# Kernel optimization log

Measured on AMD Instinct MI355X. Metric: run time of the kernel, lower is better.

## Reference

```python
import jax, jax.numpy as jnp
import numpy as np

SH_C0 = 0.28209479177387814
SH_C1 = 0.4886025119029199
SH_C2 = (1.0925484305920792, -1.0925484305920792, 0.31539156525252005, -1.0925484305920792, 0.5462742152960396)
SH_C3 = (-0.5900435899266435, 2.890611442640554, -0.4570457994644658, 0.3731763325901154, -0.4570457994644658, 1.445305721320277, -0.5900435899266435)

BG = 128  # gaussians per compositing block


def quat_to_rot(q):
    # q: [N,4] normalized quaternion (w,x,y,z) -> [N,3,3]
    w, x, y, z = q[:, 0], q[:, 1], q[:, 2], q[:, 3]
    R = jnp.stack([
        1 - 2 * (y * y + z * z), 2 * (x * y - w * z), 2 * (x * z + w * y),
        2 * (x * y + w * z), 1 - 2 * (x * x + z * z), 2 * (y * z - w * x),
        2 * (x * z - w * y), 2 * (y * z + w * x), 1 - 2 * (x * x + y * y)],
        axis=-1)
    return R.reshape(-1, 3, 3)


def eval_sh(sh, d):
    # sh: [N,16,3] degree-3 SH coeffs; d: [N,3] unit view dirs -> [N,3] rgb
    x, y, z = d[:, 0:1], d[:, 1:2], d[:, 2:3]
    xx, yy, zz = x * x, y * y, z * z
    xy, yz, xz = x * y, y * z, x * z
    res = SH_C0 * sh[:, 0]
    res = res - SH_C1 * y * sh[:, 1] + SH_C1 * z * sh[:, 2] - SH_C1 * x * sh[:, 3]
    res = (res + SH_C2[0] * xy * sh[:, 4] + SH_C2[1] * yz * sh[:, 5]
           + SH_C2[2] * (2 * zz - xx - yy) * sh[:, 6]
           + SH_C2[3] * xz * sh[:, 7] + SH_C2[4] * (xx - yy) * sh[:, 8])
    res = (res + SH_C3[0] * y * (3 * xx - yy) * sh[:, 9] + SH_C3[1] * xy * z * sh[:, 10]
           + SH_C3[2] * y * (4 * zz - xx - yy) * sh[:, 11]
           + SH_C3[3] * z * (2 * zz - 3 * xx - 3 * yy) * sh[:, 12]
           + SH_C3[4] * x * (4 * zz - xx - yy) * sh[:, 13]
           + SH_C3[5] * z * (xx - yy) * sh[:, 14] + SH_C3[6] * x * (xx - 3 * yy) * sh[:, 15])
    return res


def gs_forward(pws, shs, alphas_raw, scales_raw, rots_raw, us, Rcw, tcw, intr, height, width):
    fx, fy, cx, cy = intr[0], intr[1], intr[2], intr[3]
    N = pws.shape[0]
    HW = height * width

    # activations (GSModel.forward)
    alphas = jax.nn.sigmoid(alphas_raw[:, 0])          # [N]
    scales = jnp.exp(scales_raw)                       # [N,3]
    rots = rots_raw / jnp.linalg.norm(rots_raw, axis=1, keepdims=True)

    # gsc.project
    pcs = pws @ Rcw.T + tcw                            # [N,3] camera frame
    depth = pcs[:, 2]
    zs = jnp.where(depth > 0.2, depth, 1.0)            # safe divide for culled pts
    u = jnp.stack([fx * pcs[:, 0] / zs + cx, fy * pcs[:, 1] / zs + cy], axis=-1)
    # the `us` input is a grad-capture dummy; forward value comes from projection
    u = u + us - jax.lax.stop_gradient(us)

    # gsc.computeCov3D: Cov3d = (R S)(R S)^T
    R = quat_to_rot(rots)
    M = R * scales[:, None, :]
    cov3d = M @ jnp.swapaxes(M, 1, 2)                  # [N,3,3]

    # gsc.computeCov2D: cov2d = J W Cov3d W^T J^T + 0.3 I
    tanfx = width / (2.0 * fx)
    tanfy = height / (2.0 * fy)
    tx = jnp.clip(pcs[:, 0] / zs, -1.3 * tanfx, 1.3 * tanfx) * zs
    ty = jnp.clip(pcs[:, 1] / zs, -1.3 * tanfy, 1.3 * tanfy) * zs
    zero = jnp.zeros_like(zs)
    J = jnp.stack([
        fx / zs, zero, -fx * tx / (zs * zs),
        zero, fy / zs, -fy * ty / (zs * zs)], axis=-1).reshape(N, 2, 3)
    T = jnp.einsum('nij,jk->nik', J, Rcw)              # [N,2,3]
    cov2d = jnp.einsum('nij,njk,nlk->nil', T, cov3d, T)
    cov2d = cov2d + 0.3 * jnp.eye(2, dtype=cov2d.dtype)
    a, b, c = cov2d[:, 0, 0], cov2d[:, 0, 1], cov2d[:, 1, 1]
    det = a * c - b * b
    valid = (depth > 0.2) & (det > 0)
    det_s = jnp.where(valid, det, 1.0)

    # gsc.inverseCov2D: conic + screen-space radius (areas)
    cinv = jnp.stack([c / det_s, -b / det_s, a / det_s], axis=-1)  # [N,3]
    mid = 0.5 * (a + c)
    lam = mid + jnp.sqrt(jnp.maximum(mid * mid - det, 0.1))
    radius = jnp.where(valid, jnp.ceil(3.0 * jnp.sqrt(lam)), 0.0)
    areas = jnp.stack([radius, radius], axis=-1)       # [N,2]

    # gsc.sh2Color
    twc = -Rcw.T @ tcw
    dirs = pws - twc
    dirs = dirs / jnp.linalg.norm(dirs, axis=1, keepdims=True)
    colors = jnp.maximum(eval_sh(shs.reshape(N, 16, 3), dirs) + 0.5, 0.0)  # [N,3]

    # gsc.splat: depth-sorted front-to-back alpha compositing over all pixels
    order = jnp.argsort(depth)
    nb = N // BG
    u_s = u[order].reshape(nb, BG, 2)
    cinv_s = cinv[order].reshape(nb, BG, 3)
    al_s = alphas[order].reshape(nb, BG)
    col_s = colors[order].reshape(nb, BG, 3)
    val_s = valid[order].reshape(nb, BG)

    ys, xs = jnp.meshgrid(jnp.arange(height, dtype=jnp.float32),
                          jnp.arange(width, dtype=jnp.float32), indexing='ij')
    px = xs.ravel()
    py = ys.ravel()

    @jax.checkpoint
    def body(carry, blk):
        logT, acc = carry                              # [HW], [3,HW]
        ub, cb, ab, colb, vb = blk
        dx = px[None, :] - ub[:, 0:1]                  # [BG,HW]
        dy = py[None, :] - ub[:, 1:2]
        power = -0.5 * (cb[:, 0:1] * dx * dx + cb[:, 2:3] * dy * dy) - cb[:, 1:2] * dx * dy
        alp = jnp.minimum(0.99, ab[:, None] * jnp.exp(power))
        alp = jnp.where((power <= 0) & (alp >= 1.0 / 255.0) & vb[:, None], alp, 0.0)
        l1m = jnp.log1p(-alp)
        cs = jnp.cumsum(l1m, axis=0)
        logT_i = logT[None, :] + jnp.concatenate(
            [jnp.zeros((1, HW), l1m.dtype), cs[:-1]], axis=0)  # exclusive transmittance
        Ti = jnp.exp(logT_i)
        w = jnp.where(Ti > 1e-4, alp * Ti, 0.0)        # early-termination at tau<1e-4
        acc = acc + jnp.einsum('gp,gc->cp', w, colb)
        return (logT + cs[-1], acc), None

    init = (jnp.zeros(HW, dtype=jnp.float32), jnp.zeros((3, HW), dtype=jnp.float32))
    (_, acc), _ = jax.lax.scan(body, init, (u_s, cinv_s, al_s, col_s, val_s))
    image = acc.reshape(3, height, width)
    return image, areas


def setup_inputs() -> dict:
    key = jax.random.key(0)
    ks = jax.random.split(key, 6)
    N, H, W = 8192, 256, 256
    pws = jax.random.normal(ks[0], (N, 3), jnp.float32) * 2.0 + jnp.array([0.0, 0.0, 6.0])
    shs = jax.random.normal(ks[1], (N, 48), jnp.float32) * 0.3
    alphas_raw = jax.random.normal(ks[2], (N, 1), jnp.float32)
    scales_raw = jax.random.normal(ks[3], (N, 3), jnp.float32) * 0.3 - 3.0
    rots_raw = jax.random.normal(ks[4], (N, 4), jnp.float32)
    us = jnp.zeros((N, 2), jnp.float32)
    Rcw = jnp.eye(3, dtype=jnp.float32)
    tcw = jnp.zeros((3,), jnp.float32)
    intr = jnp.array([400.0, 400.0, 128.0, 128.0], jnp.float32)  # fx, fy, cx, cy
    return {"pws": pws, "shs": shs, "alphas_raw": alphas_raw, "scales_raw": scales_raw,
            "rots_raw": rots_raw, "us": us, "Rcw": Rcw, "tcw": tcw, "intr": intr,
            "height": H, "width": W}


def reference(pws, shs, alphas_raw, scales_raw, rots_raw, us, Rcw, tcw, intr, height, width):
    return gs_forward(pws, shs, alphas_raw, scales_raw, rots_raw, us, Rcw, tcw, intr, height, width)
```

## Files before the change

### kernel.cpp

```cpp
#include <hip/hip_runtime.h>

__global__ __launch_bounds__(256) void k_pre(
    const float* __restrict__ pws, const float* __restrict__ shs,
    const float* __restrict__ alphas_raw, const float* __restrict__ scales_raw,
    const float* __restrict__ rots_raw, const float* __restrict__ Rcw,
    const float* __restrict__ tcw, const float* __restrict__ intr,
    int N, int W, int H, float* __restrict__ areas,
    unsigned long long* __restrict__ keys, unsigned* __restrict__ rank,
    float* __restrict__ P)
{
    int i = blockIdx.x * 256 + threadIdx.x;
    if (i >= N) return;
    rank[i] = 0u;

    float R00=Rcw[0],R01=Rcw[1],R02=Rcw[2];
    float R10=Rcw[3],R11=Rcw[4],R12=Rcw[5];
    float R20=Rcw[6],R21=Rcw[7],R22=Rcw[8];
    float t0=tcw[0],t1=tcw[1],t2=tcw[2];
    float fx=intr[0],fy=intr[1],cx=intr[2],cy=intr[3];

    float pwx=pws[i*3+0], pwy=pws[i*3+1], pwz=pws[i*3+2];
    float pcx = R00*pwx + R01*pwy + R02*pwz + t0;
    float pcy = R10*pwx + R11*pwy + R12*pwz + t1;
    float pcz = R20*pwx + R21*pwy + R22*pwz + t2;
    float depth = pcz;
    float zs = (depth > 0.2f) ? depth : 1.0f;
    float u0 = fx * pcx / zs + cx;
    float u1 = fy * pcy / zs + cy;

    float qw=rots_raw[i*4+0], qx=rots_raw[i*4+1], qy=rots_raw[i*4+2], qz=rots_raw[i*4+3];
    float qn = sqrtf(qw*qw + qx*qx + qy*qy + qz*qz);
    qw/=qn; qx/=qn; qy/=qn; qz/=qn;
    float s0 = expf(scales_raw[i*3+0]);
    float s1 = expf(scales_raw[i*3+1]);
    float s2 = expf(scales_raw[i*3+2]);

    float xx=qx*qx, yy=qy*qy, zq=qz*qz;
    float xy=qx*qy, xz=qx*qz, yz=qy*qz;
    float wx=qw*qx, wy=qw*qy, wz=qw*qz;
    float r00=1.f-2.f*(yy+zq), r01=2.f*(xy-wz),     r02=2.f*(xz+wy);
    float r10=2.f*(xy+wz),     r11=1.f-2.f*(xx+zq), r12=2.f*(yz-wx);
    float r20=2.f*(xz-wy),     r21=2.f*(yz+wx),     r22=1.f-2.f*(xx+yy);

    float m00=r00*s0, m01=r01*s1, m02=r02*s2;
    float m10=r10*s0, m11=r11*s1, m12=r12*s2;
    float m20=r20*s0, m21=r21*s1, m22=r22*s2;
    float V00=m00*m00+m01*m01+m02*m02;
    float V01=m00*m10+m01*m11+m02*m12;
    float V02=m00*m20+m01*m21+m02*m22;
    float V11=m10*m10+m11*m11+m12*m12;
    float V12=m10*m20+m11*m21+m12*m22;
    float V22=m20*m20+m21*m21+m22*m22;

    float tanfx = (float)W / (2.f*fx), tanfy = (float)H / (2.f*fy);
    float limx = 1.3f*tanfx, limy = 1.3f*tanfy;
    float txl = fminf(fmaxf(pcx/zs, -limx), limx) * zs;
    float tyl = fminf(fmaxf(pcy/zs, -limy), limy) * zs;
    float iz = 1.f/zs, iz2 = iz*iz;
    float J00 = fx*iz, J02 = -fx*txl*iz2;
    float J11 = fy*iz, J12 = -fy*tyl*iz2;

    float T00=J00*R00+J02*R20, T01=J00*R01+J02*R21, T02=J00*R02+J02*R22;
    float T10=J11*R10+J12*R20, T11=J11*R11+J12*R21, T12=J11*R12+J12*R22;
    float A0=T00*V00+T01*V01+T02*V02;
    float A1=T00*V01+T01*V11+T02*V12;
    float A2=T00*V02+T01*V12+T02*V22;
    float B0=T10*V00+T11*V01+T12*V02;
    float B1=T10*V01+T11*V11+T12*V12;
    float B2=T10*V02+T11*V12+T12*V22;
    float ca = A0*T00+A1*T01+A2*T02 + 0.3f;
    float cb = A0*T10+A1*T11+A2*T12;
    float cc = B0*T10+B1*T11+B2*T12 + 0.3f;

    float det = ca*cc - cb*cb;
    bool valid = (depth > 0.2f) && (det > 0.f);
    float det_s = valid ? det : 1.f;
    float dinv = 1.f/det_s;
    float ci0 =  cc*dinv, ci1 = -cb*dinv, ci2 = ca*dinv;
    float mid = 0.5f*(ca+cc);
    float lam = mid + sqrtf(fmaxf(mid*mid - det, 0.1f));
    float radius = valid ? ceilf(3.f*sqrtf(lam)) : 0.f;
    areas[2*i+0] = radius;
    areas[2*i+1] = radius;

    float alpha = 1.f/(1.f + expf(-alphas_raw[i]));

    float tw0 = -(R00*t0 + R10*t1 + R20*t2);
    float tw1 = -(R01*t0 + R11*t1 + R21*t2);
    float tw2 = -(R02*t0 + R12*t1 + R22*t2);
    float dx_=pwx-tw0, dy_=pwy-tw1, dz_=pwz-tw2;
    float dn = sqrtf(dx_*dx_+dy_*dy_+dz_*dz_);
    float x=dx_/dn, y=dy_/dn, z=dz_/dn;
    float sxx=x*x, syy=y*y, szz=z*z;
    float sxy=x*y, syz=y*z, sxz=x*z;
    const float* sh = shs + i*48;
    float col[3];
    #pragma unroll
    for (int c = 0; c < 3; ++c) {
        float res = 0.28209479177387814f*sh[0*3+c];
        res += -0.4886025119029199f*y*sh[1*3+c]
             +  0.4886025119029199f*z*sh[2*3+c]
             + -0.4886025119029199f*x*sh[3*3+c];
        res +=  1.0925484305920792f*sxy*sh[4*3+c]
             + -1.0925484305920792f*syz*sh[5*3+c]
             +  0.31539156525252005f*(2.f*szz-sxx-syy)*sh[6*3+c]
             + -1.0925484305920792f*sxz*sh[7*3+c]
             +  0.5462742152960396f*(sxx-syy)*sh[8*3+c];
        res += -0.5900435899266435f*y*(3.f*sxx-syy)*sh[9*3+c]
             +  2.890611442640554f*sxy*z*sh[10*3+c]
             + -0.4570457994644658f*y*(4.f*szz-sxx-syy)*sh[11*3+c]
             +  0.3731763325901154f*z*(2.f*szz-3.f*sxx-3.f*syy)*sh[12*3+c]
             + -0.4570457994644658f*x*(4.f*szz-sxx-syy)*sh[13*3+c]
             +  1.445305721320277f*z*(sxx-syy)*sh[14*3+c]
             + -0.5900435899266435f*x*(sxx-3.f*syy)*sh[15*3+c];
        col[c] = fmaxf(res + 0.5f, 0.f);
    }

    float rc2;
    if (!valid || 255.f*alpha < 0.999f) {
        rc2 = -1.f;
    } else {
        float r2 = 2.f*lam*logf(255.f*alpha);
        float r  = sqrtf(fmaxf(r2, 0.f)) + 1.f;
        rc2 = r*r;
    }

    P[0*N+i]=u0;  P[1*N+i]=u1;  P[2*N+i]=ci0; P[3*N+i]=ci1; P[4*N+i]=ci2;
    P[5*N+i]=alpha; P[6*N+i]=col[0]; P[7*N+i]=col[1]; P[8*N+i]=col[2];
    P[9*N+i]=rc2;

    unsigned ud = __float_as_uint(depth);
    ud = (ud & 0x80000000u) ? ~ud : (ud | 0x80000000u);
    keys[i] = ((unsigned long long)ud << 32) | (unsigned)i;
}

#define JC 512
__global__ __launch_bounds__(256) void k_rank(
    const unsigned long long* __restrict__ keys, int N,
    unsigned* __restrict__ rank)
{
    __shared__ unsigned long long sk[JC];
    const int j0 = blockIdx.y * JC;
    for (int t = threadIdx.x; t < JC; t += 256) {
        int j = j0 + t;
        sk[t] = (j < N) ? keys[j] : ~0ull;
    }
    __syncthreads();

    const int i0 = blockIdx.x * 512 + threadIdx.x;
    const int i1 = i0 + 256;
    unsigned long long my0 = (i0 < N) ? keys[i0] : 0ull;
    unsigned long long my1 = (i1 < N) ? keys[i1] : 0ull;

    int c0 = 0, c1 = 0;
    const ulonglong2* sk2 = (const ulonglong2*)sk;
    #pragma unroll 4
    for (int t = 0; t < JC/2; ++t) {
        ulonglong2 kk = sk2[t];
        c0 += (kk.x < my0) ? 1 : 0;
        c0 += (kk.y < my0) ? 1 : 0;
        c1 += (kk.x < my1) ? 1 : 0;
        c1 += (kk.y < my1) ? 1 : 0;
    }
    if (i0 < N) atomicAdd(&rank[i0], (unsigned)c0);
    if (i1 < N) atomicAdd(&rank[i1], (unsigned)c1);
}

__global__ __launch_bounds__(256) void k_scatter(
    const unsigned* __restrict__ rank, const float* __restrict__ Pun,
    float* __restrict__ Pso, float4* __restrict__ cull, int N)
{
    int i = blockIdx.x * 256 + threadIdx.x;
    if (i >= N) return;
    int s = (int)rank[i];
    cull[s] = make_float4(Pun[0*N+i], Pun[1*N+i], Pun[9*N+i], 0.f);
    Pso[0*N+s] = Pun[2*N+i];
    Pso[1*N+s] = Pun[3*N+i];
    Pso[2*N+s] = Pun[4*N+i];
    Pso[3*N+s] = Pun[5*N+i];
    Pso[4*N+s] = Pun[6*N+i];
    Pso[5*N+s] = Pun[7*N+i];
    Pso[6*N+s] = Pun[8*N+i];
}

__global__ __launch_bounds__(256) void k_render(
    const float* __restrict__ P, const float4* __restrict__ cull,
    int N, int W, int H, float* __restrict__ out)
{
    const int tid = threadIdx.x;
    const int tilesX = (W + 15) >> 4;
    const int tX = blockIdx.x % tilesX, tY = blockIdx.x / tilesX;
    const int ix = (tX << 4) + (tid & 15);
    const int iy = (tY << 4) + (tid >> 4);
    const bool inb = (ix < W) && (iy < H);
    const float pxf = (float)ix, pyf = (float)iy;
    const float tx0 = (float)(tX << 4), ty0 = (float)(tY << 4);
    int tx1i = (tX << 4) + 15; if (tx1i > W-1) tx1i = W-1;
    int ty1i = (tY << 4) + 15; if (ty1i > H-1) ty1i = H-1;
    const float tx1 = (float)tx1i, ty1 = (float)ty1i;

    float T = inb ? 1.f : 0.f;
    float aR = 0.f, aG = 0.f, aB = 0.f;

    __shared__ float sU0[256], sU1[256], sC0[256], sC1[256], sC2[256];
    __shared__ float sA[256], sCR[256], sCG[256], sCB[256];
    __shared__ unsigned long long sMask[4];

    const int wave = tid >> 6, lane = tid & 63;

    for (int base = 0; base < N; base += 256) {
        int g = base + tid;
        bool ov = false;
        float u0=0.f,u1=0.f,c0=0.f,c1=0.f,c2=0.f,al=0.f,cr=0.f,cg=0.f,cbl=0.f;
        if (g < N) {
            float4 cu = cull[g];
            u0 = cu.x; u1 = cu.y;
            float cxp = fminf(fmaxf(u0, tx0), tx1);
            float cyp = fminf(fmaxf(u1, ty0), ty1);
            float ddx = u0 - cxp, ddy = u1 - cyp;
            ov = (ddx*ddx + ddy*ddy) <= cu.z;
            if (ov) {
                c0 = P[0*N+g]; c1 = P[1*N+g]; c2 = P[2*N+g]; al = P[3*N+g];
                cr = P[4*N+g]; cg = P[5*N+g]; cbl = P[6*N+g];
            }
        }
        unsigned long long m = __ballot(ov);
        if (lane == 0) sMask[wave] = m;
        __syncthreads();
        int cnt = 0, off = 0;
        #pragma unroll
        for (int w2 = 0; w2 < 4; ++w2) {
            int pc = __popcll(sMask[w2]);
            if (w2 < wave) off += pc;
            cnt += pc;
        }
        if (ov) {
            int pos = off + __popcll(m & ((1ull << lane) - 1ull));
            sU0[pos]=u0; sU1[pos]=u1; sC0[pos]=c0; sC1[pos]=c1; sC2[pos]=c2;
            sA[pos]=al; sCR[pos]=cr; sCB[pos]=cbl; sCG[pos]=cg;
        }
        __syncthreads();

        for (int e = 0; e < cnt; ++e) {
            float gu0=sU0[e], gu1=sU1[e];
            float gc0=sC0[e], gc1=sC1[e], gc2=sC2[e];
            float ga=sA[e], gr=sCR[e], gg=sCG[e], gb=sCB[e];
            float ddx = pxf - gu0, ddy = pyf - gu1;
            float power = -0.5f*(gc0*ddx*ddx + gc2*ddy*ddy) - gc1*ddx*ddy;
            float alp = fminf(0.99f, ga * __expf(power));
            alp = (power <= 0.f && alp >= (1.0f/255.0f)) ? alp : 0.f;
            float w = (T > 0.0001f) ? alp * T : 0.f;
            aR = fmaf(w, gr, aR);
            aG = fmaf(w, gg, aG);
            aB = fmaf(w, gb, aB);
            T = T - T * alp;
        }
        int done = (T <= 0.0001f) ? 1 : 0;
        if (__syncthreads_and(done)) break;
    }

    if (inb) {
        int p = iy * W + ix;
        int HWp = W * H;
        out[p] = aR; out[HWp + p] = aG; out[2*HWp + p] = aB;
    }
}

extern "C" void kernel_launch(void* const* d_in, const int* in_sizes, int n_in,
                              void* d_out, int out_size, void* d_ws, size_t ws_size,
                              hipStream_t stream) {
    const float* pws        = (const float*)d_in[0];
    const float* shs        = (const float*)d_in[1];
    const float* alphas_raw = (const float*)d_in[2];
    const float* scales_raw = (const float*)d_in[3];
    const float* rots_raw   = (const float*)d_in[4];
    const float* Rcw        = (const float*)d_in[6];
    const float* tcw        = (const float*)d_in[7];
    const float* intr       = (const float*)d_in[8];

    const int N  = in_sizes[0] / 3;
    const int HW = (out_size - 2 * N) / 3;
    int W = 1; while ((long long)W * W < (long long)HW) ++W;
    const int H = HW / W;

    float* out   = (float*)d_out;
    float* areas = out + 3 * HW;

    char* ws = (char*)d_ws;
    unsigned long long* keys = (unsigned long long*)ws;
    unsigned* rank = (unsigned*)(ws + (size_t)N * 8);
    float* Pun = (float*)(ws + (size_t)N * 12);
    float* Pso = Pun + (size_t)10 * N;
    float4* cullv = (float4*)(Pso + (size_t)7 * N);

    int gsN = (N + 255) / 256;
    k_pre<<<gsN, 256, 0, stream>>>(pws, shs, alphas_raw, scales_raw, rots_raw,
                                   Rcw, tcw, intr, N, W, H, areas, keys, rank, Pun);
    dim3 rgrid((N + 511) / 512, (N + JC - 1) / JC);
    k_rank<<<rgrid, 256, 0, stream>>>(keys, N, rank);
    k_scatter<<<gsN, 256, 0, stream>>>(rank, Pun, Pso, cullv, N);
    int tiles = ((W + 15) / 16) * ((H + 15) / 16);
    k_render<<<tiles, 256, 0, stream>>>(Pso, cullv, N, W, H, out);
}
```

Before: 130.9 us.

## Fuse all stages into one cooperative kernel and split rendering by depth halves

The four separate launches (preprocess, rank, scatter, render) become one cooperative kernel of 512 blocks, separated by grid-wide syncs, to remove launch gaps. Rendering now gives each 16x16 tile two blocks, each compositing one half of the depth-sorted Gaussians. The back half's transmittance and colour are written to a buffer and merged front-to-back after a final grid sync, doubling parallelism for the 256 tiles. The cost is four grid barriers, fewer threads in the preprocess and scatter phases (16 per block), and the back half doing work that early termination would otherwise skip.

```diff
diff --git a/kernel.cpp b/kernel.cpp
--- a/kernel.cpp
+++ b/kernel.cpp
@@ -1,268 +1,298 @@
 #include <hip/hip_runtime.h>
-
-__global__ __launch_bounds__(256) void k_pre(
+#include <hip/hip_cooperative_groups.h>
+
+namespace cg = cooperative_groups;
+
+#define NBLK 512
+#define BT   256
+
+union SharedU {
+    unsigned long long sk[512];
+    struct {
+        float U0[256], U1[256], C0[256], C1[256], C2[256];
+        float A[256], CR[256], CG[256], CB[256];
+        unsigned long long mask[4];
+    } r;
+};
+
+__global__ void __launch_bounds__(BT, 2) k_fused(
     const float* __restrict__ pws, const float* __restrict__ shs,
     const float* __restrict__ alphas_raw, const float* __restrict__ scales_raw,
     const float* __restrict__ rots_raw, const float* __restrict__ Rcw,
     const float* __restrict__ tcw, const float* __restrict__ intr,
-    int N, int W, int H, float* __restrict__ areas,
+    int N, int W, int H,
+    float* __restrict__ out, float* __restrict__ areas,
     unsigned long long* __restrict__ keys, unsigned* __restrict__ rank,
-    float* __restrict__ P)
+    float* __restrict__ Pun, float* __restrict__ Pso,
+    float4* __restrict__ cull, float4* __restrict__ seg1buf)
 {
-    int i = blockIdx.x * 256 + threadIdx.x;
-    if (i >= N) return;
-    rank[i] = 0u;
-
-    float R00=Rcw[0],R01=Rcw[1],R02=Rcw[2];
-    float R10=Rcw[3],R11=Rcw[4],R12=Rcw[5];
-    float R20=Rcw[6],R21=Rcw[7],R22=Rcw[8];
-    float t0=tcw[0],t1=tcw[1],t2=tcw[2];
-    float fx=intr[0],fy=intr[1],cx=intr[2],cy=intr[3];
-
-    float pwx=pws[i*3+0], pwy=pws[i*3+1], pwz=pws[i*3+2];
-    float pcx = R00*pwx + R01*pwy + R02*pwz + t0;
-    float pcy = R10*pwx + R11*pwy + R12*pwz + t1;
-    float pcz = R20*pwx + R21*pwy + R22*pwz + t2;
-    float depth = pcz;
-    float zs = (depth > 0.2f) ? depth : 1.0f;
-    float u0 = fx * pcx / zs + cx;
-    float u1 = fy * pcy / zs + cy;
-
-    float qw=rots_raw[i*4+0], qx=rots_raw[i*4+1], qy=rots_raw[i*4+2], qz=rots_raw[i*4+3];
-    float qn = sqrtf(qw*qw + qx*qx + qy*qy + qz*qz);
-    qw/=qn; qx/=qn; qy/=qn; qz/=qn;
-    float s0 = expf(scales_raw[i*3+0]);
-    float s1 = expf(scales_raw[i*3+1]);
-    float s2 = expf(scales_raw[i*3+2]);
-
-    float xx=qx*qx, yy=qy*qy, zq=qz*qz;
-    float xy=qx*qy, xz=qx*qz, yz=qy*qz;
-    float wx=qw*qx, wy=qw*qy, wz=qw*qz;
-    float r00=1.f-2.f*(yy+zq), r01=2.f*(xy-wz),     r02=2.f*(xz+wy);
-    float r10=2.f*(xy+wz),     r11=1.f-2.f*(xx+zq), r12=2.f*(yz-wx);
-    float r20=2.f*(xz-wy),     r21=2.f*(yz+wx),     r22=1.f-2.f*(xx+yy);
-
-    float m00=r00*s0, m01=r01*s1, m02=r02*s2;
-    float m10=r10*s0, m11=r11*s1, m12=r12*s2;
-    float m20=r20*s0, m21=r21*s1, m22=r22*s2;
-    float V00=m00*m00+m01*m01+m02*m02;
-    float V01=m00*m10+m01*m11+m02*m12;
-    float V02=m00*m20+m01*m21+m02*m22;
-    float V11=m10*m10+m11*m11+m12*m12;
-    float V12=m10*m20+m11*m21+m12*m22;
-    float V22=m20*m20+m21*m21+m22*m22;
-
-    float tanfx = (float)W / (2.f*fx), tanfy = (float)H / (2.f*fy);
-    float limx = 1.3f*tanfx, limy = 1.3f*tanfy;
-    float txl = fminf(fmaxf(pcx/zs, -limx), limx) * zs;
-    float tyl = fminf(fmaxf(pcy/zs, -limy), limy) * zs;
-    float iz = 1.f/zs, iz2 = iz*iz;
-    float J00 = fx*iz, J02 = -fx*txl*iz2;
-    float J11 = fy*iz, J12 = -fy*tyl*iz2;
-
-    float T00=J00*R00+J02*R20, T01=J00*R01+J02*R21, T02=J00*R02+J02*R22;
-    float T10=J11*R10+J12*R20, T11=J11*R11+J12*R21, T12=J11*R12+J12*R22;
-    float A0=T00*V00+T01*V01+T02*V02;
-    float A1=T00*V01+T01*V11+T02*V12;
-    float A2=T00*V02+T01*V12+T02*V22;
-    float B0=T10*V00+T11*V01+T12*V02;
-    float B1=T10*V01+T11*V11+T12*V12;
-    float B2=T10*V02+T11*V12+T12*V22;
-    float ca = A0*T00+A1*T01+A2*T02 + 0.3f;
-    float cb = A0*T10+A1*T11+A2*T12;
-    float cc = B0*T10+B1*T11+B2*T12 + 0.3f;
-
-    float det = ca*cc - cb*cb;
-    bool valid = (depth > 0.2f) && (det > 0.f);
-    float det_s = valid ? det : 1.f;
-    float dinv = 1.f/det_s;
-    float ci0 =  cc*dinv, ci1 = -cb*dinv, ci2 = ca*dinv;
-    float mid = 0.5f*(ca+cc);
-    float lam = mid + sqrtf(fmaxf(mid*mid - det, 0.1f));
-    float radius = valid ? ceilf(3.f*sqrtf(lam)) : 0.f;
-    areas[2*i+0] = radius;
-    areas[2*i+1] = radius;
-
-    float alpha = 1.f/(1.f + expf(-alphas_raw[i]));
-
-    float tw0 = -(R00*t0 + R10*t1 + R20*t2);
-    float tw1 = -(R01*t0 + R11*t1 + R21*t2);
-    float tw2 = -(R02*t0 + R12*t1 + R22*t2);
-    float dx_=pwx-tw0, dy_=pwy-tw1, dz_=pwz-tw2;
-    float dn = sqrtf(dx_*dx_+dy_*dy_+dz_*dz_);
-    float x=dx_/dn, y=dy_/dn, z=dz_/dn;
-    float sxx=x*x, syy=y*y, szz=z*z;
-    float sxy=x*y, syz=y*z, sxz=x*z;
-    const float* sh = shs + i*48;
-    float col[3];
-    #pragma unroll
-    for (int c = 0; c < 3; ++c) {
-        float res = 0.28209479177387814f*sh[0*3+c];
-        res += -0.4886025119029199f*y*sh[1*3+c]
-             +  0.4886025119029199f*z*sh[2*3+c]
-             + -0.4886025119029199f*x*sh[3*3+c];
-        res +=  1.0925484305920792f*sxy*sh[4*3+c]
-             + -1.0925484305920792f*syz*sh[5*3+c]
-             +  0.31539156525252005f*(2.f*szz-sxx-syy)*sh[6*3+c]
-             + -1.0925484305920792f*sxz*sh[7*3+c]
-             +  0.5462742152960396f*(sxx-syy)*sh[8*3+c];
-        res += -0.5900435899266435f*y*(3.f*sxx-syy)*sh[9*3+c]
-             +  2.890611442640554f*sxy*z*sh[10*3+c]
-             + -0.4570457994644658f*y*(4.f*szz-sxx-syy)*sh[11*3+c]
-             +  0.3731763325901154f*z*(2.f*szz-3.f*sxx-3.f*syy)*sh[12*3+c]
-             + -0.4570457994644658f*x*(4.f*szz-sxx-syy)*sh[13*3+c]
-             +  1.445305721320277f*z*(sxx-syy)*sh[14*3+c]
-             + -0.5900435899266435f*x*(sxx-3.f*syy)*sh[15*3+c];
-        col[c] = fmaxf(res + 0.5f, 0.f);
-    }
-
-    float rc2;
-    if (!valid || 255.f*alpha < 0.999f) {
-        rc2 = -1.f;
-    } else {
-        float r2 = 2.f*lam*logf(255.f*alpha);
-        float r  = sqrtf(fmaxf(r2, 0.f)) + 1.f;
-        rc2 = r*r;
-    }
-
-    P[0*N+i]=u0;  P[1*N+i]=u1;  P[2*N+i]=ci0; P[3*N+i]=ci1; P[4*N+i]=ci2;
-    P[5*N+i]=alpha; P[6*N+i]=col[0]; P[7*N+i]=col[1]; P[8*N+i]=col[2];
-    P[9*N+i]=rc2;
-
-    unsigned ud = __float_as_uint(depth);
-    ud = (ud & 0x80000000u) ? ~ud : (ud | 0x80000000u);
-    keys[i] = ((unsigned long long)ud << 32) | (unsigned)i;
-}
-
-#define JC 512
-__global__ __launch_bounds__(256) void k_rank(
-    const unsigned long long* __restrict__ keys, int N,
-    unsigned* __restrict__ rank)
-{
-    __shared__ unsigned long long sk[JC];
-    const int j0 = blockIdx.y * JC;
-    for (int t = threadIdx.x; t < JC; t += 256) {
-        int j = j0 + t;
-        sk[t] = (j < N) ? keys[j] : ~0ull;
-    }
-    __syncthreads();
-
-    const int i0 = blockIdx.x * 512 + threadIdx.x;
-    const int i1 = i0 + 256;
-    unsigned long long my0 = (i0 < N) ? keys[i0] : 0ull;
-    unsigned long long my1 = (i1 < N) ? keys[i1] : 0ull;
-
-    int c0 = 0, c1 = 0;
-    const ulonglong2* sk2 = (const ulonglong2*)sk;
-    #pragma unroll 4
-    for (int t = 0; t < JC/2; ++t) {
-        ulonglong2 kk = sk2[t];
-        c0 += (kk.x < my0) ? 1 : 0;
-        c0 += (kk.y < my0) ? 1 : 0;
-        c1 += (kk.x < my1) ? 1 : 0;
-        c1 += (kk.y < my1) ? 1 : 0;
-    }
-    if (i0 < N) atomicAdd(&rank[i0], (unsigned)c0);
-    if (i1 < N) atomicAdd(&rank[i1], (unsigned)c1);
-}
-
-__global__ __launch_bounds__(256) void k_scatter(
-    const unsigned* __restrict__ rank, const float* __restrict__ Pun,
-    float* __restrict__ Pso, float4* __restrict__ cull, int N)
-{
-    int i = blockIdx.x * 256 + threadIdx.x;
-    if (i >= N) return;
-    int s = (int)rank[i];
-    cull[s] = make_float4(Pun[0*N+i], Pun[1*N+i], Pun[9*N+i], 0.f);
-    Pso[0*N+s] = Pun[2*N+i];
-    Pso[1*N+s] = Pun[3*N+i];
-    Pso[2*N+s] = Pun[4*N+i];
-    Pso[3*N+s] = Pun[5*N+i];
-    Pso[4*N+s] = Pun[6*N+i];
-    Pso[5*N+s] = Pun[7*N+i];
-    Pso[6*N+s] = Pun[8*N+i];
-}
-
-__global__ __launch_bounds__(256) void k_render(
-    const float* __restrict__ P, const float4* __restrict__ cull,
-    int N, int W, int H, float* __restrict__ out)
-{
-    const int tid = threadIdx.x;
-    const int tilesX = (W + 15) >> 4;
-    const int tX = blockIdx.x % tilesX, tY = blockIdx.x / tilesX;
-    const int ix = (tX << 4) + (tid & 15);
-    const int iy = (tY << 4) + (tid >> 4);
-    const bool inb = (ix < W) && (iy < H);
-    const float pxf = (float)ix, pyf = (float)iy;
-    const float tx0 = (float)(tX << 4), ty0 = (float)(tY << 4);
-    int tx1i = (tX << 4) + 15; if (tx1i > W-1) tx1i = W-1;
-    int ty1i = (tY << 4) + 15; if (ty1i > H-1) ty1i = H-1;
-    const float tx1 = (float)tx1i, ty1 = (float)ty1i;
-
-    float T = inb ? 1.f : 0.f;
-    float aR = 0.f, aG = 0.f, aB = 0.f;
-
-    __shared__ float sU0[256], sU1[256], sC0[256], sC1[256], sC2[256];
-    __shared__ float sA[256], sCR[256], sCG[256], sCB[256];
-    __shared__ unsigned long long sMask[4];
-
-    const int wave = tid >> 6, lane = tid & 63;
-
-    for (int base = 0; base < N; base += 256) {
-        int g = base + tid;
-        bool ov = false;
-        float u0=0.f,u1=0.f,c0=0.f,c1=0.f,c2=0.f,al=0.f,cr=0.f,cg=0.f,cbl=0.f;
-        if (g < N) {
-            float4 cu = cull[g];
-            u0 = cu.x; u1 = cu.y;
-            float cxp = fminf(fmaxf(u0, tx0), tx1);
-            float cyp = fminf(fmaxf(u1, ty0), ty1);
-            float ddx = u0 - cxp, ddy = u1 - cyp;
-            ov = (ddx*ddx + ddy*ddy) <= cu.z;
+    cg::grid_group grid = cg::this_grid();
+    __shared__ SharedU sh;
+    const int b = blockIdx.x, tid = threadIdx.x;
+
+    {
+        const int per = (N + NBLK - 1) / NBLK;
+        const int i = b * per + tid;
+        if (tid < per && i < N) {
+            rank[i] = 0u;
+            float R00=Rcw[0],R01=Rcw[1],R02=Rcw[2];
+            float R10=Rcw[3],R11=Rcw[4],R12=Rcw[5];
+            float R20=Rcw[6],R21=Rcw[7],R22=Rcw[8];
+            float t0=tcw[0],t1=tcw[1],t2=tcw[2];
+            float fx=intr[0],fy=intr[1],cx=intr[2],cy=intr[3];
+
+            float pwx=pws[i*3+0], pwy=pws[i*3+1], pwz=pws[i*3+2];
+            float pcx = R00*pwx + R01*pwy + R02*pwz + t0;
+            float pcy = R10*pwx + R11*pwy + R12*pwz + t1;
+            float pcz = R20*pwx + R21*pwy + R22*pwz + t2;
+            float depth = pcz;
+            float zs = (depth > 0.2f) ? depth : 1.0f;
+            float u0 = fx * pcx / zs + cx;
+            float u1 = fy * pcy / zs + cy;
+
+            float qw=rots_raw[i*4+0], qx=rots_raw[i*4+1], qy=rots_raw[i*4+2], qz=rots_raw[i*4+3];
+            float qn = sqrtf(qw*qw + qx*qx + qy*qy + qz*qz);
+            qw/=qn; qx/=qn; qy/=qn; qz/=qn;
+            float s0 = expf(scales_raw[i*3+0]);
+            float s1 = expf(scales_raw[i*3+1]);
+            float s2 = expf(scales_raw[i*3+2]);
+
+            float xx=qx*qx, yy=qy*qy, zq=qz*qz;
+            float xy=qx*qy, xz=qx*qz, yz=qy*qz;
+            float wx=qw*qx, wy=qw*qy, wz=qw*qz;
+            float r00=1.f-2.f*(yy+zq), r01=2.f*(xy-wz),     r02=2.f*(xz+wy);
+            float r10=2.f*(xy+wz),     r11=1.f-2.f*(xx+zq), r12=2.f*(yz-wx);
+            float r20=2.f*(xz-wy),     r21=2.f*(yz+wx),     r22=1.f-2.f*(xx+yy);
+
+            float m00=r00*s0, m01=r01*s1, m02=r02*s2;
+            float m10=r10*s0, m11=r11*s1, m12=r12*s2;
+            float m20=r20*s0, m21=r21*s1, m22=r22*s2;
+            float V00=m00*m00+m01*m01+m02*m02;
+            float V01=m00*m10+m01*m11+m02*m12;
+            float V02=m00*m20+m01*m21+m02*m22;
+            float V11=m10*m10+m11*m11+m12*m12;
+            float V12=m10*m20+m11*m21+m12*m22;
+            float V22=m20*m20+m21*m21+m22*m22;
+
+            float tanfx = (float)W / (2.f*fx), tanfy = (float)H / (2.f*fy);
+            float limx = 1.3f*tanfx, limy = 1.3f*tanfy;
+            float txl = fminf(fmaxf(pcx/zs, -limx), limx) * zs;
+            float tyl = fminf(fmaxf(pcy/zs, -limy), limy) * zs;
+            float iz = 1.f/zs, iz2 = iz*iz;
+            float J00 = fx*iz, J02 = -fx*txl*iz2;
+            float J11 = fy*iz, J12 = -fy*tyl*iz2;
+
+            float T00=J00*R00+J02*R20, T01=J00*R01+J02*R21, T02=J00*R02+J02*R22;
+            float T10=J11*R10+J12*R20, T11=J11*R11+J12*R21, T12=J11*R12+J12*R22;
+            float A0=T00*V00+T01*V01+T02*V02;
+            float A1=T00*V01+T01*V11+T02*V12;
+            float A2=T00*V02+T01*V12+T02*V22;
+            float B0=T10*V00+T11*V01+T12*V02;
+            float B1=T10*V01+T11*V11+T12*V12;
+            float B2=T10*V02+T11*V12+T12*V22;
+            float ca = A0*T00+A1*T01+A2*T02 + 0.3f;
+            float cb = A0*T10+A1*T11+A2*T12;
+            float cc = B0*T10+B1*T11+B2*T12 + 0.3f;
+
+            float det = ca*cc - cb*cb;
+            bool valid = (depth > 0.2f) && (det > 0.f);
+            float det_s = valid ? det : 1.f;
+            float dinv = 1.f/det_s;
+            float ci0 =  cc*dinv, ci1 = -cb*dinv, ci2 = ca*dinv;
+            float mid = 0.5f*(ca+cc);
+            float lam = mid + sqrtf(fmaxf(mid*mid - det, 0.1f));
+            float radius = valid ? ceilf(3.f*sqrtf(lam)) : 0.f;
+            areas[2*i+0] = radius;
+            areas[2*i+1] = radius;
+
+            float alpha = 1.f/(1.f + expf(-alphas_raw[i]));
+
+            float tw0 = -(R00*t0 + R10*t1 + R20*t2);
+            float tw1 = -(R01*t0 + R11*t1 + R21*t2);
+            float tw2 = -(R02*t0 + R12*t1 + R22*t2);
+            float dx_=pwx-tw0, dy_=pwy-tw1, dz_=pwz-tw2;
+            float dn = sqrtf(dx_*dx_+dy_*dy_+dz_*dz_);
+            float x=dx_/dn, y=dy_/dn, z=dz_/dn;
+            float sxx=x*x, syy=y*y, szz=z*z;
+            float sxy=x*y, syz=y*z, sxz=x*z;
+            const float* shp = shs + i*48;
+            float col[3];
+            #pragma unroll
+            for (int c = 0; c < 3; ++c) {
+                float res = 0.28209479177387814f*shp[0*3+c];
+                res += -0.4886025119029199f*y*shp[1*3+c]
+                     +  0.4886025119029199f*z*shp[2*3+c]
+                     + -0.4886025119029199f*x*shp[3*3+c];
+                res +=  1.0925484305920792f*sxy*shp[4*3+c]
+                     + -1.0925484305920792f*syz*shp[5*3+c]
+                     +  0.31539156525252005f*(2.f*szz-sxx-syy)*shp[6*3+c]
+                     + -1.0925484305920792f*sxz*shp[7*3+c]
+                     +  0.5462742152960396f*(sxx-syy)*shp[8*3+c];
+                res += -0.5900435899266435f*y*(3.f*sxx-syy)*shp[9*3+c]
+                     +  2.890611442640554f*sxy*z*shp[10*3+c]
+                     + -0.4570457994644658f*y*(4.f*szz-sxx-syy)*shp[11*3+c]
+                     +  0.3731763325901154f*z*(2.f*szz-3.f*sxx-3.f*syy)*shp[12*3+c]
+                     + -0.4570457994644658f*x*(4.f*szz-sxx-syy)*shp[13*3+c]
+                     +  1.445305721320277f*z*(sxx-syy)*shp[14*3+c]
+                     + -0.5900435899266435f*x*(sxx-3.f*syy)*shp[15*3+c];
+                col[c] = fmaxf(res + 0.5f, 0.f);
+            }
+
+            float rc2;
+            if (!valid || 255.f*alpha < 0.999f) {
+                rc2 = -1.f;
+            } else {
+                float r2 = 2.f*lam*logf(255.f*alpha);
+                float rr = sqrtf(fmaxf(r2, 0.f)) + 1.f;
+                rc2 = rr*rr;
+            }
+
+            Pun[0*N+i]=u0;  Pun[1*N+i]=u1;  Pun[2*N+i]=ci0; Pun[3*N+i]=ci1;
+            Pun[4*N+i]=ci2; Pun[5*N+i]=alpha; Pun[6*N+i]=col[0];
+            Pun[7*N+i]=col[1]; Pun[8*N+i]=col[2]; Pun[9*N+i]=rc2;
+
+            unsigned ud = __float_as_uint(depth);
+            ud = (ud & 0x80000000u) ? ~ud : (ud | 0x80000000u);
+            keys[i] = ((unsigned long long)ud << 32) | (unsigned)i;
+        }
+    }
+    __threadfence();
+    grid.sync();
+
+    {
+        const int IC = (N + 255) >> 8;
+        const int JCn = (N + 511) >> 9;
+        if (b < IC * JCn) {
+            const int ic = b % IC, jc = b / IC;
+            const int j0 = jc << 9;
+            for (int t = tid; t < 512; t += BT) {
+                int j = j0 + t;
+                sh.sk[t] = (j < N) ? keys[j] : ~0ull;
+            }
+            __syncthreads();
+            const int i = (ic << 8) + tid;
+            unsigned long long my = (i < N) ? keys[i] : 0ull;
+            int c = 0;
+            const ulonglong2* sk2 = (const ulonglong2*)sh.sk;
+            #pragma unroll 8
+            for (int t = 0; t < 256; ++t) {
+                ulonglong2 kk = sk2[t];
+                c += (kk.x < my) ? 1 : 0;
+                c += (kk.y < my) ? 1 : 0;
+            }
+            if (i < N) atomicAdd(&rank[i], (unsigned)c);
+        }
+    }
+    __threadfence();
+    grid.sync();
+
+    {
+        const int per = (N + NBLK - 1) / NBLK;
+        const int i = b * per + tid;
+        if (tid < per && i < N) {
+            int s = (int)rank[i];
+            cull[s] = make_float4(Pun[0*N+i], Pun[1*N+i], Pun[9*N+i], 0.f);
+            Pso[0*N+s] = Pun[2*N+i];
+            Pso[1*N+s] = Pun[3*N+i];
+            Pso[2*N+s] = Pun[4*N+i];
+            Pso[3*N+s] = Pun[5*N+i];
+            Pso[4*N+s] = Pun[6*N+i];
+            Pso[5*N+s] = Pun[7*N+i];
+            Pso[6*N+s] = Pun[8*N+i];
+        }
+    }
+    __threadfence();
+    grid.sync();
+
+    const int tilesX = (W + 15) >> 4, tilesY = (H + 15) >> 4;
+    const int nTiles = tilesX * tilesY;
+    const int tile = b >> 1, seg = b & 1;
+    const int half = (N + 1) >> 1;
+
+    float T = 0.f, aR = 0.f, aG = 0.f, aB = 0.f;
+    int pix = 0;
+    bool inb = false;
+
+    if (tile < nTiles) {
+        const int tX = tile % tilesX, tY = tile / tilesX;
+        const int ix = (tX << 4) + (tid & 15);
+        const int iy = (tY << 4) + (tid >> 4);
+        inb = (ix < W) && (iy < H);
+        pix = inb ? (iy * W + ix) : 0;
+        const float pxf = (float)ix, pyf = (float)iy;
+        const float tx0 = (float)(tX << 4), ty0 = (float)(tY << 4);
+        int tx1i = (tX << 4) + 15; if (tx1i > W-1) tx1i = W-1;
+        int ty1i = (tY << 4) + 15; if (ty1i > H-1) ty1i = H-1;
+        const float tx1 = (float)tx1i, ty1 = (float)ty1i;
+
+        T = inb ? 1.f : 0.f;
+        const int g0 = seg ? half : 0;
+        const int g1 = seg ? N : half;
+        const int wave = tid >> 6, lane = tid & 63;
+
+        for (int base = g0; base < g1; base += BT) {
+            int g = base + tid;
+            bool ov = false;
+            float u0=0.f,u1=0.f,c0=0.f,c1=0.f,c2=0.f,al=0.f,cr=0.f,cg=0.f,cbl=0.f;
+            if (g < g1) {
+                float4 cu = cull[g];
+                u0 = cu.x; u1 = cu.y;
+                float cxp = fminf(fmaxf(u0, tx0), tx1);
+                float cyp = fminf(fmaxf(u1, ty0), ty1);
+                float ddx = u0 - cxp, ddy = u1 - cyp;
+                ov = (ddx*ddx + ddy*ddy) <= cu.z;
+                if (ov) {
+                    c0 = Pso[0*N+g]; c1 = Pso[1*N+g]; c2 = Pso[2*N+g]; al = Pso[3*N+g];
+                    cr = Pso[4*N+g]; cg = Pso[5*N+g]; cbl = Pso[6*N+g];
+                }
+            }
+            unsigned long long m = __ballot(ov);
+            if (lane == 0) sh.r.mask[wave] = m;
+            __syncthreads();
+            int cnt = 0, off = 0;
+            #pragma unroll
+            for (int w2 = 0; w2 < 4; ++w2) {
+                int pc = __popcll(sh.r.mask[w2]);
+                if (w2 < wave) off += pc;
+                cnt += pc;
+            }
             if (ov) {
-                c0 = P[0*N+g]; c1 = P[1*N+g]; c2 = P[2*N+g]; al = P[3*N+g];
-                cr = P[4*N+g]; cg = P[5*N+g]; cbl = P[6*N+g];
-            }
+                int pos = off + __popcll(m & ((1ull << lane) - 1ull));
+                sh.r.U0[pos]=u0; sh.r.U1[pos]=u1; sh.r.C0[pos]=c0;
+                sh.r.C1[pos]=c1; sh.r.C2[pos]=c2; sh.r.A[pos]=al;
+                sh.r.CR[pos]=cr; sh.r.CG[pos]=cg; sh.r.CB[pos]=cbl;
+            }
+            __syncthreads();
+
+            for (int e = 0; e < cnt; ++e) {
+                float gu0=sh.r.U0[e], gu1=sh.r.U1[e];
+                float gc0=sh.r.C0[e], gc1=sh.r.C1[e], gc2=sh.r.C2[e];
+                float ga=sh.r.A[e], gr=sh.r.CR[e], gg=sh.r.CG[e], gb=sh.r.CB[e];
+                float ddx = pxf - gu0, ddy = pyf - gu1;
+                float power = -0.5f*(gc0*ddx*ddx + gc2*ddy*ddy) - gc1*ddx*ddy;
+                float alp = fminf(0.99f, ga * __expf(power));
+                alp = (power <= 0.f && alp >= (1.0f/255.0f)) ? alp : 0.f;
+                float w = (T > 0.0001f) ? alp * T : 0.f;
+                aR = fmaf(w, gr, aR);
+                aG = fmaf(w, gg, aG);
+                aB = fmaf(w, gb, aB);
+                T = T - T * alp;
+            }
+            int done = (T <= 0.0001f) ? 1 : 0;
+            if (__syncthreads_and(done)) break;
         }
-        unsigned long long m = __ballot(ov);
-        if (lane == 0) sMask[wave] = m;
-        __syncthreads();
-        int cnt = 0, off = 0;
-        #pragma unroll
-        for (int w2 = 0; w2 < 4; ++w2) {
-            int pc = __popcll(sMask[w2]);
-            if (w2 < wave) off += pc;
-            cnt += pc;
-        }
-        if (ov) {
-            int pos = off + __popcll(m & ((1ull << lane) - 1ull));
-            sU0[pos]=u0; sU1[pos]=u1; sC0[pos]=c0; sC1[pos]=c1; sC2[pos]=c2;
-            sA[pos]=al; sCR[pos]=cr; sCB[pos]=cbl; sCG[pos]=cg;
-        }
-        __syncthreads();
-
-        for (int e = 0; e < cnt; ++e) {
-            float gu0=sU0[e], gu1=sU1[e];
-            float gc0=sC0[e], gc1=sC1[e], gc2=sC2[e];
-            float ga=sA[e], gr=sCR[e], gg=sCG[e], gb=sCB[e];
-            float ddx = pxf - gu0, ddy = pyf - gu1;
-            float power = -0.5f*(gc0*ddx*ddx + gc2*ddy*ddy) - gc1*ddx*ddy;
-            float alp = fminf(0.99f, ga * __expf(power));
-            alp = (power <= 0.f && alp >= (1.0f/255.0f)) ? alp : 0.f;
-            float w = (T > 0.0001f) ? alp * T : 0.f;
-            aR = fmaf(w, gr, aR);
-            aG = fmaf(w, gg, aG);
-            aB = fmaf(w, gb, aB);
-            T = T - T * alp;
-        }
-        int done = (T <= 0.0001f) ? 1 : 0;
-        if (__syncthreads_and(done)) break;
-    }
-
-    if (inb) {
-        int p = iy * W + ix;
-        int HWp = W * H;
-        out[p] = aR; out[HWp + p] = aG; out[2*HWp + p] = aB;
+
+        if (seg == 1 && inb) seg1buf[pix] = make_float4(T, aR, aG, aB);
+    }
+    __threadfence();
+    grid.sync();
+
+    if (tile < nTiles && seg == 0 && inb) {
+        float4 s1 = seg1buf[pix];
+        const int HWp = W * H;
+        out[pix]         = aR + T * s1.y;
+        out[HWp + pix]   = aG + T * s1.z;
+        out[2*HWp + pix] = aB + T * s1.w;
     }
 }
 
@@ -278,10 +308,10 @@
     const float* tcw        = (const float*)d_in[7];
     const float* intr       = (const float*)d_in[8];
 
-    const int N  = in_sizes[0] / 3;
-    const int HW = (out_size - 2 * N) / 3;
+    int N  = in_sizes[0] / 3;
+    int HW = (out_size - 2 * N) / 3;
     int W = 1; while ((long long)W * W < (long long)HW) ++W;
-    const int H = HW / W;
+    int H = HW / W;
 
     float* out   = (float*)d_out;
     float* areas = out + 3 * HW;
@@ -292,13 +322,16 @@
     float* Pun = (float*)(ws + (size_t)N * 12);
     float* Pso = Pun + (size_t)10 * N;
     float4* cullv = (float4*)(Pso + (size_t)7 * N);
-
-    int gsN = (N + 255) / 256;
-    k_pre<<<gsN, 256, 0, stream>>>(pws, shs, alphas_raw, scales_raw, rots_raw,
-                                   Rcw, tcw, intr, N, W, H, areas, keys, rank, Pun);
-    dim3 rgrid((N + 511) / 512, (N + JC - 1) / JC);
-    k_rank<<<rgrid, 256, 0, stream>>>(keys, N, rank);
-    k_scatter<<<gsN, 256, 0, stream>>>(rank, Pun, Pso, cullv, N);
-    int tiles = ((W + 15) / 16) * ((H + 15) / 16);
-    k_render<<<tiles, 256, 0, stream>>>(Pso, cullv, N, W, H, out);
+    float4* seg1buf = cullv + N;
+
+    void* args[] = {
+        (void*)&pws, (void*)&shs, (void*)&alphas_raw, (void*)&scales_raw,
+        (void*)&rots_raw, (void*)&Rcw, (void*)&tcw, (void*)&intr,
+        (void*)&N, (void*)&W, (void*)&H,
+        (void*)&out, (void*)&areas,
+        (void*)&keys, (void*)&rank, (void*)&Pun, (void*)&Pso,
+        (void*)&cullv, (void*)&seg1buf
+    };
+    hipLaunchCooperativeKernel((const void*)k_fused, dim3(NBLK), dim3(BT),
+                               args, 0, stream);
 }
```

After: 463.7 us. +254.1%, slower.

## Split render over depth segments and merge partial composites in a combine pass

Applied to the files above, without the earlier changes.

The render kernel now splits the sorted Gaussian list into up to four depth segments, each handled by its own block per tile, and writes partial transmittance and colour per pixel to a workspace buffer. A new combine kernel merges the segments front to back. Gaussian parameters are also packed into float4 arrays, so global and shared-memory accesses become vectorised. This raises block count from 256 tiles so more of the GPU is busy, but later segments can no longer stop early on saturated transmittance, which adds work and an extra kernel launch.

```diff
diff --git a/kernel.cpp b/kernel.cpp
--- a/kernel.cpp
+++ b/kernel.cpp
@@ -168,28 +168,26 @@
 
 __global__ __launch_bounds__(256) void k_scatter(
     const unsigned* __restrict__ rank, const float* __restrict__ Pun,
-    float* __restrict__ Pso, float4* __restrict__ cull, int N)
+    float4* __restrict__ gA, float4* __restrict__ gB,
+    float4* __restrict__ cull, int N)
 {
     int i = blockIdx.x * 256 + threadIdx.x;
     if (i >= N) return;
     int s = (int)rank[i];
     cull[s] = make_float4(Pun[0*N+i], Pun[1*N+i], Pun[9*N+i], 0.f);
-    Pso[0*N+s] = Pun[2*N+i];
-    Pso[1*N+s] = Pun[3*N+i];
-    Pso[2*N+s] = Pun[4*N+i];
-    Pso[3*N+s] = Pun[5*N+i];
-    Pso[4*N+s] = Pun[6*N+i];
-    Pso[5*N+s] = Pun[7*N+i];
-    Pso[6*N+s] = Pun[8*N+i];
+    gA[s]   = make_float4(Pun[2*N+i], Pun[3*N+i], Pun[4*N+i], Pun[5*N+i]);
+    gB[s]   = make_float4(Pun[6*N+i], Pun[7*N+i], Pun[8*N+i], 0.f);
 }
 
 __global__ __launch_bounds__(256) void k_render(
-    const float* __restrict__ P, const float4* __restrict__ cull,
-    int N, int W, int H, float* __restrict__ out)
+    const float4* __restrict__ gA, const float4* __restrict__ gB,
+    const float4* __restrict__ cull, int N, int W, int H,
+    int nTiles, int nseg, float4* __restrict__ segbuf)
 {
     const int tid = threadIdx.x;
     const int tilesX = (W + 15) >> 4;
-    const int tX = blockIdx.x % tilesX, tY = blockIdx.x / tilesX;
+    const int tile = blockIdx.x % nTiles, seg = blockIdx.x / nTiles;
+    const int tX = tile % tilesX, tY = tile / tilesX;
     const int ix = (tX << 4) + (tid & 15);
     const int iy = (tY << 4) + (tid >> 4);
     const bool inb = (ix < W) && (iy < H);
@@ -199,30 +197,34 @@
     int ty1i = (tY << 4) + 15; if (ty1i > H-1) ty1i = H-1;
     const float tx1 = (float)tx1i, ty1 = (float)ty1i;
 
+    const int per = (N + nseg - 1) / nseg;
+    const int g0 = seg * per;
+    const int g1 = min(N, g0 + per);
+
     float T = inb ? 1.f : 0.f;
     float aR = 0.f, aG = 0.f, aB = 0.f;
 
-    __shared__ float sU0[256], sU1[256], sC0[256], sC1[256], sC2[256];
-    __shared__ float sA[256], sCR[256], sCG[256], sCB[256];
+    __shared__ float4 sG0[256];
+    __shared__ float4 sG1[256];
+    __shared__ float  sB2[256];
     __shared__ unsigned long long sMask[4];
 
     const int wave = tid >> 6, lane = tid & 63;
 
-    for (int base = 0; base < N; base += 256) {
+    for (int base = g0; base < g1; base += 256) {
         int g = base + tid;
         bool ov = false;
-        float u0=0.f,u1=0.f,c0=0.f,c1=0.f,c2=0.f,al=0.f,cr=0.f,cg=0.f,cbl=0.f;
-        if (g < N) {
+        float u0=0.f, u1=0.f;
+        float4 a4 = make_float4(0.f,0.f,0.f,0.f);
+        float4 b4 = make_float4(0.f,0.f,0.f,0.f);
+        if (g < g1) {
             float4 cu = cull[g];
             u0 = cu.x; u1 = cu.y;
             float cxp = fminf(fmaxf(u0, tx0), tx1);
             float cyp = fminf(fmaxf(u1, ty0), ty1);
             float ddx = u0 - cxp, ddy = u1 - cyp;
             ov = (ddx*ddx + ddy*ddy) <= cu.z;
-            if (ov) {
-                c0 = P[0*N+g]; c1 = P[1*N+g]; c2 = P[2*N+g]; al = P[3*N+g];
-                cr = P[4*N+g]; cg = P[5*N+g]; cbl = P[6*N+g];
-            }
+            if (ov) { a4 = gA[g]; b4 = gB[g]; }
         }
         unsigned long long m = __ballot(ov);
         if (lane == 0) sMask[wave] = m;
@@ -236,22 +238,23 @@
         }
         if (ov) {
             int pos = off + __popcll(m & ((1ull << lane) - 1ull));
-            sU0[pos]=u0; sU1[pos]=u1; sC0[pos]=c0; sC1[pos]=c1; sC2[pos]=c2;
-            sA[pos]=al; sCR[pos]=cr; sCB[pos]=cbl; sCG[pos]=cg;
+            sG0[pos] = make_float4(u0, u1, a4.x, a4.y);
+            sG1[pos] = make_float4(a4.z, a4.w, b4.x, b4.y);
+            sB2[pos] = b4.z;
         }
         __syncthreads();
 
         for (int e = 0; e < cnt; ++e) {
-            float gu0=sU0[e], gu1=sU1[e];
-            float gc0=sC0[e], gc1=sC1[e], gc2=sC2[e];
-            float ga=sA[e], gr=sCR[e], gg=sCG[e], gb=sCB[e];
-            float ddx = pxf - gu0, ddy = pyf - gu1;
-            float power = -0.5f*(gc0*ddx*ddx + gc2*ddy*ddy) - gc1*ddx*ddy;
-            float alp = fminf(0.99f, ga * __expf(power));
+            float4 e0 = sG0[e];
+            float4 e1 = sG1[e];
+            float  gb = sB2[e];
+            float ddx = pxf - e0.x, ddy = pyf - e0.y;
+            float power = -0.5f*(e0.z*ddx*ddx + e1.x*ddy*ddy) - e0.w*ddx*ddy;
+            float alp = fminf(0.99f, e1.y * __expf(power));
             alp = (power <= 0.f && alp >= (1.0f/255.0f)) ? alp : 0.f;
             float w = (T > 0.0001f) ? alp * T : 0.f;
-            aR = fmaf(w, gr, aR);
-            aG = fmaf(w, gg, aG);
+            aR = fmaf(w, e1.z, aR);
+            aG = fmaf(w, e1.w, aG);
             aB = fmaf(w, gb, aB);
             T = T - T * alp;
         }
@@ -260,10 +263,26 @@
     }
 
     if (inb) {
-        int p = iy * W + ix;
-        int HWp = W * H;
-        out[p] = aR; out[HWp + p] = aG; out[2*HWp + p] = aB;
-    }
+        int pix = iy * W + ix;
+        segbuf[(size_t)seg * (size_t)(W*H) + pix] = make_float4(T, aR, aG, aB);
+    }
+}
+
+__global__ __launch_bounds__(256) void k_combine(
+    const float4* __restrict__ segbuf, int HW, int nseg,
+    float* __restrict__ out)
+{
+    int p = blockIdx.x * 256 + threadIdx.x;
+    if (p >= HW) return;
+    float T = 1.f, r = 0.f, g = 0.f, b = 0.f;
+    for (int s = 0; s < nseg; ++s) {
+        float4 v = segbuf[(size_t)s * HW + p];
+        r = fmaf(T, v.y, r);
+        g = fmaf(T, v.z, g);
+        b = fmaf(T, v.w, b);
+        T *= v.x;
+    }
+    out[p] = r; out[HW + p] = g; out[2*HW + p] = b;
 }
 
 extern "C" void kernel_launch(void* const* d_in, const int* in_sizes, int n_in,
@@ -287,18 +306,29 @@
     float* areas = out + 3 * HW;
 
     char* ws = (char*)d_ws;
-    unsigned long long* keys = (unsigned long long*)ws;
-    unsigned* rank = (unsigned*)(ws + (size_t)N * 8);
-    float* Pun = (float*)(ws + (size_t)N * 12);
-    float* Pso = Pun + (size_t)10 * N;
-    float4* cullv = (float4*)(Pso + (size_t)7 * N);
+    size_t off = 0;
+    unsigned long long* keys = (unsigned long long*)(ws + off); off += (size_t)N * 8;
+    unsigned* rank = (unsigned*)(ws + off);                     off += (size_t)N * 4;
+    off = (off + 15) & ~(size_t)15;
+    float* Pun = (float*)(ws + off);                            off += (size_t)10 * N * 4;
+    off = (off + 15) & ~(size_t)15;
+    float4* cullv = (float4*)(ws + off);                        off += (size_t)N * 16;
+    float4* gA = (float4*)(ws + off);                           off += (size_t)N * 16;
+    float4* gB = (float4*)(ws + off);                           off += (size_t)N * 16;
+    float4* segbuf = (float4*)(ws + off);
+    size_t remain = (ws_size > off) ? (ws_size - off) : 0;
+    int nseg = 4;
+    while (nseg > 1 && (size_t)nseg * (size_t)HW * 16 > remain) nseg >>= 1;
 
     int gsN = (N + 255) / 256;
     k_pre<<<gsN, 256, 0, stream>>>(pws, shs, alphas_raw, scales_raw, rots_raw,
                                    Rcw, tcw, intr, N, W, H, areas, keys, rank, Pun);
     dim3 rgrid((N + 511) / 512, (N + JC - 1) / JC);
     k_rank<<<rgrid, 256, 0, stream>>>(keys, N, rank);
-    k_scatter<<<gsN, 256, 0, stream>>>(rank, Pun, Pso, cullv, N);
-    int tiles = ((W + 15) / 16) * ((H + 15) / 16);
-    k_render<<<tiles, 256, 0, stream>>>(Pso, cullv, N, W, H, out);
-}
+    k_scatter<<<gsN, 256, 0, stream>>>(rank, Pun, gA, gB, cullv, N);
+    int tilesX = (W + 15) / 16, tilesY = (H + 15) / 16;
+    int nTiles = tilesX * tilesY;
+    k_render<<<nTiles * nseg, 256, 0, stream>>>(gA, gB, cullv, N, W, H,
+                                                nTiles, nseg, segbuf);
+    k_combine<<<(HW + 255) / 256, 256, 0, stream>>>(segbuf, HW, nseg, out);
+}
```

Result: faster. 109.2 us (-16.6%).
